# Optimization experiments

Hardware: AMD Instinct MI355X
Metric: run time of the kernel (lower is better)

Reference implementation:

```python
import jax, jax.numpy as jnp
import numpy as np

D_IN, D_HIDDEN, D_OUT, BATCH = 128, 512, 128, 65536


def setup_inputs() -> dict:
    key = jax.random.key(0)
    k_x, k_u, k_a, k_b, k_c = jax.random.split(key, 5)
    return {
        "x": jax.random.normal(k_x, (BATCH, D_HIDDEN), dtype=jnp.float32),
        "u": jax.random.normal(k_u, (BATCH, D_IN), dtype=jnp.float32),
        "a": jax.random.normal(k_a, (D_HIDDEN,), dtype=jnp.float32),
        "b": jax.random.normal(k_b, (D_IN, D_HIDDEN), dtype=jnp.float32),
        "c": jax.random.normal(k_c, (D_HIDDEN, D_OUT), dtype=jnp.float32),
    }


def reference(x, u, a, b, c):
    # Diagonal linear RNN step: new state = decay * x + u @ b, then output GEMM.
    decay = jax.nn.softmax(a)  # [d_hidden]
    x_new = x * decay[None, :] + u @ b  # [B, d_hidden]
    output = x_new @ c  # [B, d_out]
    return (x_new, output)
```

## Files before the change

### kernel.cpp

```cpp
#include <hip/hip_runtime.h>
#include <hip/hip_bf16.h>

#define BATCH 65536
#define DIN   128
#define DH    512
#define DOUT  128
#define ROWS  32

typedef __attribute__((ext_vector_type(4))) float f32x4;
typedef __attribute__((ext_vector_type(8))) short s16x8;

__device__ __forceinline__ ushort f32_to_bf16_rn(float f) {
    uint32_t u = __float_as_uint(f);
    uint32_t r = (u + 0x7FFFu + ((u >> 16) & 1u)) >> 16;
    return (ushort)r;
}
__device__ __forceinline__ float bf16_to_f32(ushort h) {
    return __uint_as_float(((uint32_t)h) << 16);
}

__device__ __forceinline__ f32x4 mfma16(s16x8 a, s16x8 b, f32x4 c) {
    return __builtin_amdgcn_mfma_f32_16x16x32_bf16(a, b, c, 0, 0, 0);
}

struct Split8 { s16x8 h, l; };
__device__ __forceinline__ Split8 split8(f32x4 v0, f32x4 v1) {
    Split8 s;
#pragma unroll
    for (int j = 0; j < 4; ++j) {
        ushort hh = f32_to_bf16_rn(v0[j]);
        s.h[j] = (short)hh;
        s.l[j] = (short)f32_to_bf16_rn(v0[j] - bf16_to_f32(hh));
    }
#pragma unroll
    for (int j = 0; j < 4; ++j) {
        ushort hh = f32_to_bf16_rn(v1[j]);
        s.h[4 + j] = (short)hh;
        s.l[4 + j] = (short)f32_to_bf16_rn(v1[j] - bf16_to_f32(hh));
    }
    return s;
}

__global__ void prep_kernel(const float* __restrict__ a,
                            const float* __restrict__ b,
                            const float* __restrict__ c,
                            float* __restrict__ decay,
                            ushort* __restrict__ bhi, ushort* __restrict__ blo,
                            ushort* __restrict__ chi, ushort* __restrict__ clo)
{
    const int t = threadIdx.x;
    if (blockIdx.x == 0) {
        __shared__ float red[256];
        float v0 = a[t], v1 = a[t + 256];
        red[t] = fmaxf(v0, v1);
        __syncthreads();
        for (int s = 128; s > 0; s >>= 1) {
            if (t < s) red[t] = fmaxf(red[t], red[t + s]);
            __syncthreads();
        }
        float M = red[0];
        __syncthreads();
        float e0 = expf(v0 - M), e1 = expf(v1 - M);
        red[t] = e0 + e1;
        __syncthreads();
        for (int s = 128; s > 0; s >>= 1) {
            if (t < s) red[t] += red[t + s];
            __syncthreads();
        }
        float S = red[0];
        decay[t]       = e0 / S;
        decay[t + 256] = e1 / S;
    } else {
        const int p = (blockIdx.x - 1) * 256 + t;
        const int mtx = p >> 13;
        const int q = p & 8191;
        const int f = q >> 6;
        const int l = q & 63;
        s16x8 hi, lo;
        if (mtx == 0) {
            const int cg = f >> 2, ks = f & 3;
            const int col = cg * 16 + (l & 15);
            const int kbase = ks * 32 + (l >> 4) * 8;
#pragma unroll
            for (int j = 0; j < 8; ++j) {
                float v = b[(size_t)(kbase + j) * DH + col];
                ushort h = f32_to_bf16_rn(v);
                hi[j] = (short)h;
                lo[j] = (short)f32_to_bf16_rn(v - bf16_to_f32(h));
            }
            *(s16x8*)(bhi + (size_t)q * 8) = hi;
            *(s16x8*)(blo + (size_t)q * 8) = lo;
        } else {
            const int cg = f >> 4, ks = f & 15;
            const int col = cg * 16 + (l & 15);
            const int kbase = ks * 32 + (l >> 4) * 8;
#pragma unroll
            for (int j = 0; j < 8; ++j) {
                float v = c[(size_t)(kbase + j) * DOUT + col];
                ushort h = f32_to_bf16_rn(v);
                hi[j] = (short)h;
                lo[j] = (short)f32_to_bf16_rn(v - bf16_to_f32(h));
            }
            *(s16x8*)(chi + (size_t)q * 8) = hi;
            *(s16x8*)(clo + (size_t)q * 8) = lo;
        }
    }
}

__global__ __launch_bounds__(256, 4)
void rnn_fused(const float* __restrict__ u, const float* __restrict__ x,
               const float* __restrict__ decay,
               const ushort* __restrict__ bhi, const ushort* __restrict__ blo,
               const ushort* __restrict__ chi, const ushort* __restrict__ clo,
               float* __restrict__ xn, float* __restrict__ out)
{
    __shared__ __align__(16) char smem[24576];
    ushort* Ah = (ushort*)smem;
    ushort* Al = (ushort*)(smem + 8192);
    ushort* Xh = (ushort*)(smem + 16384);
    ushort* Xl = (ushort*)(smem + 20480);

    const int t = threadIdx.x;
    const int lane = t & 63, wc = t >> 6;
    const int cl = lane & 15, hk = lane >> 4;
    const int row0 = blockIdx.x * ROWS;

    {
        const int r = t >> 3;
        const int kb = (t & 7) * 2;
#pragma unroll
        for (int i = 0; i < 2; ++i) {
            const float* src = u + (size_t)(row0 + r) * DIN + (kb + i) * 8;
            f32x4 v0 = *(const f32x4*)src;
            f32x4 v1 = *(const f32x4*)(src + 4);
            Split8 s = split8(v0, v1);
            const int byte = (r * 256 + (kb + i) * 16) ^ ((r & 7) << 4);
            *(s16x8*)((char*)Ah + byte) = s.h;
            *(s16x8*)((char*)Al + byte) = s.l;
        }
    }
    __syncthreads();

    f32x4 acc2[2][2];
#pragma unroll
    for (int mf = 0; mf < 2; ++mf)
#pragma unroll
        for (int nf = 0; nf < 2; ++nf)
            acc2[mf][nf] = (f32x4){0.f, 0.f, 0.f, 0.f};

    for (int ct = 0; ct < 8; ++ct) {
        const int col = ct * 64 + wc * 16 + cl;
        const float dv = decay[col];
        float xv[2][4];
#pragma unroll
        for (int mf = 0; mf < 2; ++mf)
#pragma unroll
            for (int j = 0; j < 4; ++j)
                xv[mf][j] = x[(size_t)(row0 + mf * 16 + hk * 4 + j) * DH + col];

        f32x4 acc1[2];
        acc1[0] = (f32x4){0.f, 0.f, 0.f, 0.f};
        acc1[1] = (f32x4){0.f, 0.f, 0.f, 0.f};
#pragma unroll
        for (int ks = 0; ks < 4; ++ks) {
            const int ko = ks * 32 + hk * 8;
            s16x8 ah[2], al[2];
#pragma unroll
            for (int mf = 0; mf < 2; ++mf) {
                const int r = mf * 16 + cl;
                const int byte = (r * 256 + ko * 2) ^ ((r & 7) << 4);
                ah[mf] = *(const s16x8*)((const char*)Ah + byte);
                al[mf] = *(const s16x8*)((const char*)Al + byte);
            }
            const size_t fB = (size_t)((ct * 4 + wc) * 4 + ks) * 512 + lane * 8;
            s16x8 bh = *(const s16x8*)(bhi + fB);
            s16x8 bl = *(const s16x8*)(blo + fB);
#pragma unroll
            for (int mf = 0; mf < 2; ++mf) acc1[mf] = mfma16(ah[mf], bh, acc1[mf]);
#pragma unroll
            for (int mf = 0; mf < 2; ++mf) acc1[mf] = mfma16(ah[mf], bl, acc1[mf]);
#pragma unroll
            for (int mf = 0; mf < 2; ++mf) acc1[mf] = mfma16(al[mf], bh, acc1[mf]);
        }

        __syncthreads();

#pragma unroll
        for (int mf = 0; mf < 2; ++mf) {
#pragma unroll
            for (int j = 0; j < 4; ++j) {
                const int rl = mf * 16 + hk * 4 + j;
                const float v = acc1[mf][j] + dv * xv[mf][j];
                xn[(size_t)(row0 + rl) * DH + col] = v;
                const ushort hh = f32_to_bf16_rn(v);
                const ushort ll = f32_to_bf16_rn(v - bf16_to_f32(hh));
                const int cbyte = (rl * 128 + (wc * 16 + cl) * 2) ^ ((rl & 7) << 4);
                *(ushort*)((char*)Xh + cbyte) = hh;
                *(ushort*)((char*)Xl + cbyte) = ll;
            }
        }
        __syncthreads();

#pragma unroll
        for (int ks2 = 0; ks2 < 2; ++ks2) {
            const int ko = ks2 * 32 + hk * 8;
            s16x8 ah2[2], al2[2];
#pragma unroll
            for (int mf = 0; mf < 2; ++mf) {
                const int r = mf * 16 + cl;
                const int byte = (r * 128 + ko * 2) ^ ((r & 7) << 4);
                ah2[mf] = *(const s16x8*)((const char*)Xh + byte);
                al2[mf] = *(const s16x8*)((const char*)Xl + byte);
            }
#pragma unroll
            for (int nf = 0; nf < 2; ++nf) {
                const size_t fC = (size_t)((wc * 2 + nf) * 16 + ct * 2 + ks2) * 512 + lane * 8;
                s16x8 ch = *(const s16x8*)(chi + fC);
                s16x8 cc = *(const s16x8*)(clo + fC);
#pragma unroll
                for (int mf = 0; mf < 2; ++mf) acc2[mf][nf] = mfma16(ah2[mf], ch, acc2[mf][nf]);
#pragma unroll
                for (int mf = 0; mf < 2; ++mf) acc2[mf][nf] = mfma16(ah2[mf], cc, acc2[mf][nf]);
#pragma unroll
                for (int mf = 0; mf < 2; ++mf) acc2[mf][nf] = mfma16(al2[mf], ch, acc2[mf][nf]);
            }
        }
    }

#pragma unroll
    for (int nf = 0; nf < 2; ++nf) {
        const int ocol = wc * 32 + nf * 16 + cl;
#pragma unroll
        for (int mf = 0; mf < 2; ++mf) {
#pragma unroll
            for (int j = 0; j < 4; ++j) {
                const int rl = mf * 16 + hk * 4 + j;
                out[(size_t)(row0 + rl) * DOUT + ocol] = acc2[mf][nf][j];
            }
        }
    }
}

extern "C" void kernel_launch(void* const* d_in, const int* in_sizes, int n_in,
                              void* d_out, int out_size, void* d_ws, size_t ws_size,
                              hipStream_t stream)
{
    const float* x = (const float*)d_in[0];
    const float* u = (const float*)d_in[1];
    const float* a = (const float*)d_in[2];
    const float* b = (const float*)d_in[3];
    const float* c = (const float*)d_in[4];

    float* xn  = (float*)d_out;
    float* out = xn + (size_t)BATCH * DH;

    float*  decay = (float*)d_ws;
    ushort* bhi = (ushort*)((char*)d_ws + 4096);
    ushort* blo = bhi + 128 * 512;
    ushort* chi = blo + 128 * 512;
    ushort* clo = chi + 512 * 128;

    prep_kernel<<<dim3(65), dim3(256), 0, stream>>>(a, b, c, decay, bhi, blo, chi, clo);
    rnn_fused<<<dim3(BATCH / ROWS), dim3(256), 0, stream>>>(u, x, decay, bhi, blo, chi, clo, xn, out);
}
```

Baseline: 113.0 us.

## Split hidden dim across waves with split-K reduction for the output GEMM

Each wave now owns 128 hidden columns for the whole first GEMM, reading u fragments straight from global memory into registers instead of staging them through shared memory. It then does a partial second GEMM over its own hidden slice into a full 32x128 accumulator, and the four waves' partials are reduced through shared memory before coalesced vector stores of the output. This removes the per-column-tile block barriers and the shared A staging. In exchange register pressure rises (occupancy hint drops from 4 to 3), u is read redundantly by every wave, and a serial cross-wave reduction with several barriers is added at the end.

```diff
diff --git a/kernel.cpp b/kernel.cpp
--- a/kernel.cpp
+++ b/kernel.cpp
@@ -107,138 +107,161 @@
     }
 }
 
-__global__ __launch_bounds__(256, 4)
+__global__ __launch_bounds__(256, 3)
 void rnn_fused(const float* __restrict__ u, const float* __restrict__ x,
                const float* __restrict__ decay,
                const ushort* __restrict__ bhi, const ushort* __restrict__ blo,
                const ushort* __restrict__ chi, const ushort* __restrict__ clo,
                float* __restrict__ xn, float* __restrict__ out)
 {
-    __shared__ __align__(16) char smem[24576];
-    ushort* Ah = (ushort*)smem;
-    ushort* Al = (ushort*)(smem + 8192);
-    ushort* Xh = (ushort*)(smem + 16384);
-    ushort* Xl = (ushort*)(smem + 20480);
-
+    __shared__ __align__(16) char smem[32768];
     const int t = threadIdx.x;
-    const int lane = t & 63, wc = t >> 6;
+    const int lane = t & 63, w = t >> 6;
     const int cl = lane & 15, hk = lane >> 4;
     const int row0 = blockIdx.x * ROWS;
-
-    {
-        const int r = t >> 3;
-        const int kb = (t & 7) * 2;
-#pragma unroll
-        for (int i = 0; i < 2; ++i) {
-            const float* src = u + (size_t)(row0 + r) * DIN + (kb + i) * 8;
+    const int wcol = w * 128;
+
+    char* Xh = smem + w * 8192;
+    char* Xl = smem + w * 8192 + 4096;
+
+    float dv[8];
+#pragma unroll
+    for (int nf = 0; nf < 8; ++nf) dv[nf] = decay[wcol + nf * 16 + cl];
+
+    f32x4 acc1[2][8];
+#pragma unroll
+    for (int mf = 0; mf < 2; ++mf)
+#pragma unroll
+        for (int nf = 0; nf < 8; ++nf)
+            acc1[mf][nf] = (f32x4){0.f, 0.f, 0.f, 0.f};
+
+#pragma unroll
+    for (int ks = 0; ks < 4; ++ks) {
+        s16x8 auh[2], aul[2];
+#pragma unroll
+        for (int mf = 0; mf < 2; ++mf) {
+            const float* src = u + (size_t)(row0 + mf * 16 + cl) * DIN + ks * 32 + hk * 8;
             f32x4 v0 = *(const f32x4*)src;
             f32x4 v1 = *(const f32x4*)(src + 4);
             Split8 s = split8(v0, v1);
-            const int byte = (r * 256 + (kb + i) * 16) ^ ((r & 7) << 4);
-            *(s16x8*)((char*)Ah + byte) = s.h;
-            *(s16x8*)((char*)Al + byte) = s.l;
-        }
-    }
-    __syncthreads();
-
-    f32x4 acc2[2][2];
-#pragma unroll
-    for (int mf = 0; mf < 2; ++mf)
-#pragma unroll
-        for (int nf = 0; nf < 2; ++nf)
-            acc2[mf][nf] = (f32x4){0.f, 0.f, 0.f, 0.f};
-
-    for (int ct = 0; ct < 8; ++ct) {
-        const int col = ct * 64 + wc * 16 + cl;
-        const float dv = decay[col];
-        float xv[2][4];
-#pragma unroll
-        for (int mf = 0; mf < 2; ++mf)
-#pragma unroll
-            for (int j = 0; j < 4; ++j)
-                xv[mf][j] = x[(size_t)(row0 + mf * 16 + hk * 4 + j) * DH + col];
-
-        f32x4 acc1[2];
-        acc1[0] = (f32x4){0.f, 0.f, 0.f, 0.f};
-        acc1[1] = (f32x4){0.f, 0.f, 0.f, 0.f};
-#pragma unroll
-        for (int ks = 0; ks < 4; ++ks) {
-            const int ko = ks * 32 + hk * 8;
-            s16x8 ah[2], al[2];
-#pragma unroll
-            for (int mf = 0; mf < 2; ++mf) {
-                const int r = mf * 16 + cl;
-                const int byte = (r * 256 + ko * 2) ^ ((r & 7) << 4);
-                ah[mf] = *(const s16x8*)((const char*)Ah + byte);
-                al[mf] = *(const s16x8*)((const char*)Al + byte);
-            }
-            const size_t fB = (size_t)((ct * 4 + wc) * 4 + ks) * 512 + lane * 8;
+            auh[mf] = s.h;
+            aul[mf] = s.l;
+        }
+#pragma unroll
+        for (int nf = 0; nf < 8; ++nf) {
+            const size_t fB = (size_t)((w * 8 + nf) * 4 + ks) * 512 + lane * 8;
             s16x8 bh = *(const s16x8*)(bhi + fB);
             s16x8 bl = *(const s16x8*)(blo + fB);
 #pragma unroll
-            for (int mf = 0; mf < 2; ++mf) acc1[mf] = mfma16(ah[mf], bh, acc1[mf]);
-#pragma unroll
-            for (int mf = 0; mf < 2; ++mf) acc1[mf] = mfma16(ah[mf], bl, acc1[mf]);
-#pragma unroll
-            for (int mf = 0; mf < 2; ++mf) acc1[mf] = mfma16(al[mf], bh, acc1[mf]);
-        }
-
-        __syncthreads();
-
-#pragma unroll
-        for (int mf = 0; mf < 2; ++mf) {
-#pragma unroll
-            for (int j = 0; j < 4; ++j) {
-                const int rl = mf * 16 + hk * 4 + j;
-                const float v = acc1[mf][j] + dv * xv[mf][j];
-                xn[(size_t)(row0 + rl) * DH + col] = v;
-                const ushort hh = f32_to_bf16_rn(v);
-                const ushort ll = f32_to_bf16_rn(v - bf16_to_f32(hh));
-                const int cbyte = (rl * 128 + (wc * 16 + cl) * 2) ^ ((rl & 7) << 4);
-                *(ushort*)((char*)Xh + cbyte) = hh;
-                *(ushort*)((char*)Xl + cbyte) = ll;
-            }
-        }
-        __syncthreads();
-
+            for (int mf = 0; mf < 2; ++mf) acc1[mf][nf] = mfma16(auh[mf], bh, acc1[mf][nf]);
+#pragma unroll
+            for (int mf = 0; mf < 2; ++mf) acc1[mf][nf] = mfma16(auh[mf], bl, acc1[mf][nf]);
+#pragma unroll
+            for (int mf = 0; mf < 2; ++mf) acc1[mf][nf] = mfma16(aul[mf], bh, acc1[mf][nf]);
+        }
+    }
+
+    f32x4 acc2[2][8];
+#pragma unroll
+    for (int mf = 0; mf < 2; ++mf)
+#pragma unroll
+        for (int nf = 0; nf < 8; ++nf)
+            acc2[mf][nf] = (f32x4){0.f, 0.f, 0.f, 0.f};
+
+#pragma unroll
+    for (int half = 0; half < 2; ++half) {
+#pragma unroll
+        for (int nfh = 0; nfh < 4; ++nfh) {
+            const int nf = half * 4 + nfh;
+            const int col = wcol + nf * 16 + cl;
+#pragma unroll
+            for (int mf = 0; mf < 2; ++mf) {
+#pragma unroll
+                for (int j = 0; j < 4; ++j) {
+                    const int lrow = mf * 16 + 4 * hk + j;
+                    const size_t gidx = (size_t)(row0 + lrow) * DH + col;
+                    const float v = acc1[mf][nf][j] + dv[nf] * x[gidx];
+                    xn[gidx] = v;
+                    const ushort hh = f32_to_bf16_rn(v);
+                    const ushort ll = f32_to_bf16_rn(v - bf16_to_f32(hh));
+                    const int cb = (lrow * 128 + (nfh * 16 + cl) * 2) ^ ((lrow & 7) << 4);
+                    *(ushort*)(Xh + cb) = hh;
+                    *(ushort*)(Xl + cb) = ll;
+                }
+            }
+        }
 #pragma unroll
         for (int ks2 = 0; ks2 < 2; ++ks2) {
-            const int ko = ks2 * 32 + hk * 8;
-            s16x8 ah2[2], al2[2];
+            s16x8 xh[2], xl[2];
 #pragma unroll
             for (int mf = 0; mf < 2; ++mf) {
-                const int r = mf * 16 + cl;
-                const int byte = (r * 128 + ko * 2) ^ ((r & 7) << 4);
-                ah2[mf] = *(const s16x8*)((const char*)Xh + byte);
-                al2[mf] = *(const s16x8*)((const char*)Xl + byte);
-            }
-#pragma unroll
-            for (int nf = 0; nf < 2; ++nf) {
-                const size_t fC = (size_t)((wc * 2 + nf) * 16 + ct * 2 + ks2) * 512 + lane * 8;
+                const int lrow = mf * 16 + cl;
+                const int cb = (lrow * 128 + (ks2 * 32 + hk * 8) * 2) ^ ((lrow & 7) << 4);
+                xh[mf] = *(const s16x8*)(Xh + cb);
+                xl[mf] = *(const s16x8*)(Xl + cb);
+            }
+            const int ksg = w * 4 + half * 2 + ks2;
+#pragma unroll
+            for (int nf2 = 0; nf2 < 8; ++nf2) {
+                const size_t fC = (size_t)(nf2 * 16 + ksg) * 512 + lane * 8;
                 s16x8 ch = *(const s16x8*)(chi + fC);
                 s16x8 cc = *(const s16x8*)(clo + fC);
 #pragma unroll
-                for (int mf = 0; mf < 2; ++mf) acc2[mf][nf] = mfma16(ah2[mf], ch, acc2[mf][nf]);
-#pragma unroll
-                for (int mf = 0; mf < 2; ++mf) acc2[mf][nf] = mfma16(ah2[mf], cc, acc2[mf][nf]);
-#pragma unroll
-                for (int mf = 0; mf < 2; ++mf) acc2[mf][nf] = mfma16(al2[mf], ch, acc2[mf][nf]);
-            }
-        }
-    }
-
-#pragma unroll
-    for (int nf = 0; nf < 2; ++nf) {
-        const int ocol = wc * 32 + nf * 16 + cl;
-#pragma unroll
-        for (int mf = 0; mf < 2; ++mf) {
-#pragma unroll
-            for (int j = 0; j < 4; ++j) {
-                const int rl = mf * 16 + hk * 4 + j;
-                out[(size_t)(row0 + rl) * DOUT + ocol] = acc2[mf][nf][j];
-            }
-        }
-    }
+                for (int mf = 0; mf < 2; ++mf) acc2[mf][nf2] = mfma16(xh[mf], ch, acc2[mf][nf2]);
+#pragma unroll
+                for (int mf = 0; mf < 2; ++mf) acc2[mf][nf2] = mfma16(xh[mf], cc, acc2[mf][nf2]);
+#pragma unroll
+                for (int mf = 0; mf < 2; ++mf) acc2[mf][nf2] = mfma16(xl[mf], ch, acc2[mf][nf2]);
+            }
+        }
+    }
+
+    float* R = (float*)smem;
+
+#define STORE_ACC(DST)                                                        \
+    {                                                                         \
+        _Pragma("unroll")                                                     \
+        for (int mf = 0; mf < 2; ++mf)                                        \
+            _Pragma("unroll")                                                 \
+            for (int nf2 = 0; nf2 < 8; ++nf2)                                 \
+                _Pragma("unroll")                                             \
+                for (int j = 0; j < 4; ++j)                                   \
+                    (DST)[(mf * 16 + 4 * hk + j) * 128 + nf2 * 16 + cl] =     \
+                        acc2[mf][nf2][j];                                     \
+    }
+#define ADD_ACC(SRC)                                                          \
+    {                                                                         \
+        _Pragma("unroll")                                                     \
+        for (int mf = 0; mf < 2; ++mf)                                        \
+            _Pragma("unroll")                                                 \
+            for (int nf2 = 0; nf2 < 8; ++nf2)                                 \
+                _Pragma("unroll")                                             \
+                for (int j = 0; j < 4; ++j)                                   \
+                    acc2[mf][nf2][j] +=                                       \
+                        (SRC)[(mf * 16 + 4 * hk + j) * 128 + nf2 * 16 + cl];  \
+    }
+
+    __syncthreads();
+    if (w == 1) STORE_ACC(R);
+    if (w == 3) STORE_ACC(R + 4096);
+    __syncthreads();
+    if (w == 0) ADD_ACC(R);
+    if (w == 2) ADD_ACC(R + 4096);
+    __syncthreads();
+    if (w == 2) STORE_ACC(R);
+    __syncthreads();
+    if (w == 0) { ADD_ACC(R); STORE_ACC(R); }
+    __syncthreads();
+
+#pragma unroll
+    for (int i = 0; i < 4; ++i) {
+        const int slot = t + i * 256;
+        const int r = slot >> 5, seg = slot & 31;
+        *(f32x4*)&out[(size_t)(row0 + r) * DOUT + seg * 4] =
+            *(const f32x4*)&R[r * 128 + seg * 4];
+    }
+#undef STORE_ACC
+#undef ADD_ACC
 }
 
 extern "C" void kernel_launch(void* const* d_in, const int* in_sizes, int n_in,
```

Measured after the change: 321.5 us. +184.5%, slower.

## Decouple output GEMM from state via precomputed B·C and double-buffered decayed X

Applied to the files above, without the earlier changes.

Rewrites output = (decay*x)@C + u@(B@C), with B@C precomputed in a new prep kernel and split into bf16 hi/lo. The second GEMM now consumes decay*x, which is available before the first GEMM, so the two GEMMs no longer depend on each other. This removes one __syncthreads per tile, double-buffers the X LDS tile, and prefetches the next x/decay tile. The cost is an extra small GEMM (K=128) at the end, two more prep launches, a naive B@C product, and a duplicated LDS store loop. The reassociation also changes floating-point rounding.

```diff
diff --git a/kernel.cpp b/kernel.cpp
--- a/kernel.cpp
+++ b/kernel.cpp
@@ -18,7 +18,6 @@
 __device__ __forceinline__ float bf16_to_f32(ushort h) {
     return __uint_as_float(((uint32_t)h) << 16);
 }
-
 __device__ __forceinline__ f32x4 mfma16(s16x8 a, s16x8 b, f32x4 c) {
     return __builtin_amdgcn_mfma_f32_16x16x32_bf16(a, b, c, 0, 0, 0);
 }
@@ -41,12 +40,20 @@
     return s;
 }
 
-__global__ void prep_kernel(const float* __restrict__ a,
-                            const float* __restrict__ b,
-                            const float* __restrict__ c,
-                            float* __restrict__ decay,
-                            ushort* __restrict__ bhi, ushort* __restrict__ blo,
-                            ushort* __restrict__ chi, ushort* __restrict__ clo)
+#define LGKM_BARRIER()                                              \
+    do {                                                            \
+        __builtin_amdgcn_sched_barrier(0);                          \
+        asm volatile("s_waitcnt lgkmcnt(0)\n\ts_barrier" ::: "memory"); \
+        __builtin_amdgcn_sched_barrier(0);                          \
+    } while (0)
+
+__global__ void prep1_kernel(const float* __restrict__ a,
+                             const float* __restrict__ b,
+                             const float* __restrict__ c,
+                             float* __restrict__ decay,
+                             ushort* __restrict__ bhi, ushort* __restrict__ blo,
+                             ushort* __restrict__ chi, ushort* __restrict__ clo,
+                             float* __restrict__ bcf)
 {
     const int t = threadIdx.x;
     if (blockIdx.x == 0) {
@@ -70,7 +77,7 @@
         float S = red[0];
         decay[t]       = e0 / S;
         decay[t + 256] = e1 / S;
-    } else {
+    } else if (blockIdx.x <= 64) {
         const int p = (blockIdx.x - 1) * 256 + t;
         const int mtx = p >> 13;
         const int q = p & 8191;
@@ -104,7 +111,34 @@
             *(s16x8*)(chi + (size_t)q * 8) = hi;
             *(s16x8*)(clo + (size_t)q * 8) = lo;
         }
-    }
+    } else {
+        const int i = (blockIdx.x - 65) * 2 + (t >> 7);
+        const int j = t & 127;
+        float acc = 0.f;
+        for (int k = 0; k < DH; ++k)
+            acc = fmaf(b[(size_t)i * DH + k], c[(size_t)k * DOUT + j], acc);
+        bcf[i * DOUT + j] = acc;
+    }
+}
+
+__global__ void prep2_kernel(const float* __restrict__ bcf,
+                             ushort* __restrict__ bch, ushort* __restrict__ bcl)
+{
+    const int p = blockIdx.x * 256 + threadIdx.x;
+    const int f = p >> 6, l = p & 63;
+    const int cg = f >> 2, ks = f & 3;
+    const int col = cg * 16 + (l & 15);
+    const int kbase = ks * 32 + (l >> 4) * 8;
+    s16x8 hi, lo;
+#pragma unroll
+    for (int j = 0; j < 8; ++j) {
+        float v = bcf[(size_t)(kbase + j) * DOUT + col];
+        ushort h = f32_to_bf16_rn(v);
+        hi[j] = (short)h;
+        lo[j] = (short)f32_to_bf16_rn(v - bf16_to_f32(h));
+    }
+    *(s16x8*)(bch + (size_t)p * 8) = hi;
+    *(s16x8*)(bcl + (size_t)p * 8) = lo;
 }
 
 __global__ __launch_bounds__(256, 4)
@@ -112,16 +146,15 @@
                const float* __restrict__ decay,
                const ushort* __restrict__ bhi, const ushort* __restrict__ blo,
                const ushort* __restrict__ chi, const ushort* __restrict__ clo,
+               const ushort* __restrict__ bch, const ushort* __restrict__ bcl,
                float* __restrict__ xn, float* __restrict__ out)
 {
-    __shared__ __align__(16) char smem[24576];
+    __shared__ __align__(16) char smem[32768];
     ushort* Ah = (ushort*)smem;
     ushort* Al = (ushort*)(smem + 8192);
-    ushort* Xh = (ushort*)(smem + 16384);
-    ushort* Xl = (ushort*)(smem + 20480);
 
     const int t = threadIdx.x;
-    const int lane = t & 63, wc = t >> 6;
+    const int lane = t & 63, w = t >> 6;
     const int cl = lane & 15, hk = lane >> 4;
     const int row0 = blockIdx.x * ROWS;
 
@@ -139,6 +172,15 @@
             *(s16x8*)((char*)Al + byte) = s.l;
         }
     }
+
+    float xv[2][4], xvn[2][4], dvc, dvn;
+    dvc = decay[w * 16 + cl];
+#pragma unroll
+    for (int mf = 0; mf < 2; ++mf)
+#pragma unroll
+        for (int j = 0; j < 4; ++j)
+            xv[mf][j] = x[(size_t)(row0 + mf * 16 + 4 * hk + j) * DH + w * 16 + cl];
+
     __syncthreads();
 
     f32x4 acc2[2][2];
@@ -149,14 +191,45 @@
             acc2[mf][nf] = (f32x4){0.f, 0.f, 0.f, 0.f};
 
     for (int ct = 0; ct < 8; ++ct) {
-        const int col = ct * 64 + wc * 16 + cl;
-        const float dv = decay[col];
-        float xv[2][4];
-#pragma unroll
-        for (int mf = 0; mf < 2; ++mf)
-#pragma unroll
-            for (int j = 0; j < 4; ++j)
-                xv[mf][j] = x[(size_t)(row0 + mf * 16 + hk * 4 + j) * DH + col];
+        char* Xh = smem + 16384 + (ct & 1) * 8192;
+        char* Xl = Xh + 4096;
+
+#pragma unroll
+        for (int mf = 0; mf < 2; ++mf) {
+#pragma unroll
+            for (int j = 0; j < 4; ++j) {
+                const float v = dvc * xv[mf][j];
+                const int lrow = mf * 16 + 4 * hk + j;
+                const int cb = (lrow * 128 + (w * 16 + cl) * 2) ^ ((lrow & 7) << 4);
+                *(ushort*)(Xh + cb) = f32_to_bf16_rn(v);
+                *(ushort*)(Xl + cb) = f32_to_bf16_rn(v - bf16_to_f32(__float_as_uint(v) >> 16 ? f32_to_bf16_rn(v) : f32_to_bf16_rn(v)));
+            }
+        }
+#pragma unroll
+        for (int mf = 0; mf < 2; ++mf) {
+#pragma unroll
+            for (int j = 0; j < 4; ++j) {
+                const float v = dvc * xv[mf][j];
+                const ushort hh = f32_to_bf16_rn(v);
+                const ushort ll = f32_to_bf16_rn(v - bf16_to_f32(hh));
+                const int lrow = mf * 16 + 4 * hk + j;
+                const int cb = (lrow * 128 + (w * 16 + cl) * 2) ^ ((lrow & 7) << 4);
+                *(ushort*)(Xh + cb) = hh;
+                *(ushort*)(Xl + cb) = ll;
+            }
+        }
+
+        if (ct < 7) {
+            const int ncol = (ct + 1) * 64 + w * 16 + cl;
+            dvn = decay[ncol];
+#pragma unroll
+            for (int mf = 0; mf < 2; ++mf)
+#pragma unroll
+                for (int j = 0; j < 4; ++j)
+                    xvn[mf][j] = x[(size_t)(row0 + mf * 16 + 4 * hk + j) * DH + ncol];
+        }
+
+        LGKM_BARRIER();
 
         f32x4 acc1[2];
         acc1[0] = (f32x4){0.f, 0.f, 0.f, 0.f};
@@ -172,7 +245,7 @@
                 ah[mf] = *(const s16x8*)((const char*)Ah + byte);
                 al[mf] = *(const s16x8*)((const char*)Al + byte);
             }
-            const size_t fB = (size_t)((ct * 4 + wc) * 4 + ks) * 512 + lane * 8;
+            const size_t fB = (size_t)((ct * 4 + w) * 4 + ks) * 512 + lane * 8;
             s16x8 bh = *(const s16x8*)(bhi + fB);
             s16x8 bl = *(const s16x8*)(blo + fB);
 #pragma unroll
@@ -183,61 +256,82 @@
             for (int mf = 0; mf < 2; ++mf) acc1[mf] = mfma16(al[mf], bh, acc1[mf]);
         }
 
-        __syncthreads();
-
-#pragma unroll
-        for (int mf = 0; mf < 2; ++mf) {
-#pragma unroll
-            for (int j = 0; j < 4; ++j) {
-                const int rl = mf * 16 + hk * 4 + j;
-                const float v = acc1[mf][j] + dv * xv[mf][j];
-                xn[(size_t)(row0 + rl) * DH + col] = v;
-                const ushort hh = f32_to_bf16_rn(v);
-                const ushort ll = f32_to_bf16_rn(v - bf16_to_f32(hh));
-                const int cbyte = (rl * 128 + (wc * 16 + cl) * 2) ^ ((rl & 7) << 4);
-                *(ushort*)((char*)Xh + cbyte) = hh;
-                *(ushort*)((char*)Xl + cbyte) = ll;
-            }
-        }
-        __syncthreads();
-
 #pragma unroll
         for (int ks2 = 0; ks2 < 2; ++ks2) {
-            const int ko = ks2 * 32 + hk * 8;
-            s16x8 ah2[2], al2[2];
+            s16x8 xh[2], xl[2];
 #pragma unroll
             for (int mf = 0; mf < 2; ++mf) {
-                const int r = mf * 16 + cl;
-                const int byte = (r * 128 + ko * 2) ^ ((r & 7) << 4);
-                ah2[mf] = *(const s16x8*)((const char*)Xh + byte);
-                al2[mf] = *(const s16x8*)((const char*)Xl + byte);
-            }
-#pragma unroll
-            for (int nf = 0; nf < 2; ++nf) {
-                const size_t fC = (size_t)((wc * 2 + nf) * 16 + ct * 2 + ks2) * 512 + lane * 8;
+                const int lrow = mf * 16 + cl;
+                const int cb = (lrow * 128 + (ks2 * 32 + hk * 8) * 2) ^ ((lrow & 7) << 4);
+                xh[mf] = *(const s16x8*)(Xh + cb);
+                xl[mf] = *(const s16x8*)(Xl + cb);
+            }
+            const int ksg = ct * 2 + ks2;
+#pragma unroll
+            for (int nf2 = 0; nf2 < 2; ++nf2) {
+                const size_t fC = (size_t)((w * 2 + nf2) * 16 + ksg) * 512 + lane * 8;
                 s16x8 ch = *(const s16x8*)(chi + fC);
                 s16x8 cc = *(const s16x8*)(clo + fC);
 #pragma unroll
-                for (int mf = 0; mf < 2; ++mf) acc2[mf][nf] = mfma16(ah2[mf], ch, acc2[mf][nf]);
-#pragma unroll
-                for (int mf = 0; mf < 2; ++mf) acc2[mf][nf] = mfma16(ah2[mf], cc, acc2[mf][nf]);
-#pragma unroll
-                for (int mf = 0; mf < 2; ++mf) acc2[mf][nf] = mfma16(al2[mf], ch, acc2[mf][nf]);
-            }
-        }
-    }
-
-#pragma unroll
-    for (int nf = 0; nf < 2; ++nf) {
-        const int ocol = wc * 32 + nf * 16 + cl;
+                for (int mf = 0; mf < 2; ++mf) acc2[mf][nf2] = mfma16(xh[mf], ch, acc2[mf][nf2]);
+#pragma unroll
+                for (int mf = 0; mf < 2; ++mf) acc2[mf][nf2] = mfma16(xh[mf], cc, acc2[mf][nf2]);
+#pragma unroll
+                for (int mf = 0; mf < 2; ++mf) acc2[mf][nf2] = mfma16(xl[mf], ch, acc2[mf][nf2]);
+            }
+        }
+
+        {
+            const int col = ct * 64 + w * 16 + cl;
+#pragma unroll
+            for (int mf = 0; mf < 2; ++mf)
+#pragma unroll
+                for (int j = 0; j < 4; ++j)
+                    xn[(size_t)(row0 + mf * 16 + 4 * hk + j) * DH + col] =
+                        acc1[mf][j] + dvc * xv[mf][j];
+        }
+
+        dvc = dvn;
+#pragma unroll
+        for (int mf = 0; mf < 2; ++mf)
+#pragma unroll
+            for (int j = 0; j < 4; ++j) xv[mf][j] = xvn[mf][j];
+    }
+
+#pragma unroll
+    for (int ks = 0; ks < 4; ++ks) {
+        const int ko = ks * 32 + hk * 8;
+        s16x8 ah[2], al[2];
 #pragma unroll
         for (int mf = 0; mf < 2; ++mf) {
-#pragma unroll
-            for (int j = 0; j < 4; ++j) {
-                const int rl = mf * 16 + hk * 4 + j;
-                out[(size_t)(row0 + rl) * DOUT + ocol] = acc2[mf][nf][j];
-            }
-        }
+            const int r = mf * 16 + cl;
+            const int byte = (r * 256 + ko * 2) ^ ((r & 7) << 4);
+            ah[mf] = *(const s16x8*)((const char*)Ah + byte);
+            al[mf] = *(const s16x8*)((const char*)Al + byte);
+        }
+#pragma unroll
+        for (int nf2 = 0; nf2 < 2; ++nf2) {
+            const size_t fbc = (size_t)((w * 2 + nf2) * 4 + ks) * 512 + lane * 8;
+            s16x8 h2 = *(const s16x8*)(bch + fbc);
+            s16x8 l2 = *(const s16x8*)(bcl + fbc);
+#pragma unroll
+            for (int mf = 0; mf < 2; ++mf) acc2[mf][nf2] = mfma16(ah[mf], h2, acc2[mf][nf2]);
+#pragma unroll
+            for (int mf = 0; mf < 2; ++mf) acc2[mf][nf2] = mfma16(ah[mf], l2, acc2[mf][nf2]);
+#pragma unroll
+            for (int mf = 0; mf < 2; ++mf) acc2[mf][nf2] = mfma16(al[mf], h2, acc2[mf][nf2]);
+        }
+    }
+
+#pragma unroll
+    for (int nf2 = 0; nf2 < 2; ++nf2) {
+        const int ocol = w * 32 + nf2 * 16 + cl;
+#pragma unroll
+        for (int mf = 0; mf < 2; ++mf)
+#pragma unroll
+            for (int j = 0; j < 4; ++j)
+                out[(size_t)(row0 + mf * 16 + 4 * hk + j) * DOUT + ocol] =
+                    acc2[mf][nf2][j];
     }
 }
 
@@ -254,12 +348,17 @@
     float* xn  = (float*)d_out;
     float* out = xn + (size_t)BATCH * DH;
 
-    float*  decay = (float*)d_ws;
-    ushort* bhi = (ushort*)((char*)d_ws + 4096);
+    char* ws = (char*)d_ws;
+    float*  decay = (float*)ws;
+    ushort* bhi = (ushort*)(ws + 4096);
     ushort* blo = bhi + 128 * 512;
     ushort* chi = blo + 128 * 512;
     ushort* clo = chi + 512 * 128;
-
-    prep_kernel<<<dim3(65), dim3(256), 0, stream>>>(a, b, c, decay, bhi, blo, chi, clo);
-    rnn_fused<<<dim3(BATCH / ROWS), dim3(256), 0, stream>>>(u, x, decay, bhi, blo, chi, clo, xn, out);
-}
+    float*  bcf = (float*)(ws + 4096 + 4 * 131072);
+    ushort* bch = (ushort*)(ws + 4096 + 4 * 131072 + 65536);
+    ushort* bcl = bch + 128 * 128;
+
+    prep1_kernel<<<dim3(129), dim3(256), 0, stream>>>(a, b, c, decay, bhi, blo, chi, clo, bcf);
+    prep2_kernel<<<dim3(8), dim3(256), 0, stream>>>(bcf, bch, bcl);
+    rnn_fused<<<dim3(BATCH / ROWS), dim3(256), 0, stream>>>(u, x, decay, bhi, blo, chi, clo, bch, bcl, xn, out);
+}
```

Measured after the change: 149.5 us. 1.32x slower.
